# Optimization experiments

Hardware: AMD Instinct MI355X
Metric: run time of the kernel (lower is better)

## Reference

```python
import jax, jax.numpy as jnp
import numpy as np

N_USER = 100000
N_ITEM = 150000
N = N_USER + N_ITEM
D = 64            # latdim
NNZ = 1250000     # sparse adjacency nnz
BATCH = 16384     # node_ids batch
NUM_GNN_LAYERS = 2
GD = 16           # gate_dim (mamba d_model)
DSTATE = 8
DCONV = 4
EXPAND = 2
DINNER = GD * EXPAND  # 32
DTRANK = 1            # ceil(GD/16)
TEMP = 0.8            # gate_temp


def setup_inputs() -> dict:
    key = jax.random.key(0)
    ks = jax.random.split(key, 20)
    f32 = jnp.float32
    inp = {}
    inp["user_embedding"] = jax.random.normal(ks[0], (N_USER, D), f32) * 0.02
    inp["item_embedding"] = jax.random.normal(ks[1], (N_ITEM, D), f32) * 0.02
    inp["edge_row"] = jax.random.randint(ks[2], (NNZ,), 0, N, dtype=jnp.int32)
    inp["edge_col"] = jax.random.randint(ks[3], (NNZ,), 0, N, dtype=jnp.int32)
    inp["edge_val"] = jax.random.uniform(ks[4], (NNZ,), f32) * 0.1
    inp["node_ids"] = jax.random.randint(ks[5], (BATCH,), 0, N, dtype=jnp.int32)
    # gate params (torch Linear weight layout: [out, in])
    inp["down_w"] = jax.random.normal(ks[6], (GD, D), f32) * 0.02
    inp["in_proj_w"] = jax.random.normal(ks[7], (2 * DINNER, GD), f32) * 0.05
    inp["conv_w"] = jax.random.normal(ks[8], (DINNER, DCONV), f32) * 0.1
    inp["conv_b"] = jnp.zeros((DINNER,), f32)
    inp["x_proj_w"] = jax.random.normal(ks[9], (DTRANK + 2 * DSTATE, DINNER), f32) * 0.05
    inp["dt_proj_w"] = jax.random.normal(ks[10], (DINNER, DTRANK), f32) * 0.1
    inp["dt_proj_b"] = jax.random.normal(ks[11], (DINNER,), f32) * 0.1
    inp["A_log"] = jnp.log(jnp.broadcast_to(jnp.arange(1, DSTATE + 1, dtype=f32), (DINNER, DSTATE)))
    inp["D_param"] = jnp.ones((DINNER,), f32)
    inp["out_proj_w"] = jax.random.normal(ks[12], (GD, DINNER), f32) * 0.05
    inp["ln_g"] = jnp.ones((GD,), f32)
    inp["ln_b"] = jnp.zeros((GD,), f32)
    inp["to_logit_w"] = jax.random.normal(ks[13], (1, GD), f32) * 0.02
    inp["to_logit_b"] = jnp.zeros((1,), f32)
    return inp


def _mamba(g, in_proj_w, conv_w, conv_b, x_proj_w, dt_proj_w, dt_proj_b, A_log, D_param, out_proj_w):
    # g: [B, L, GD] -- standard Mamba block (selective scan)
    Bsz, L, _ = g.shape
    xz = g @ in_proj_w.T                     # [B,L,2*DINNER]
    x, z = jnp.split(xz, 2, axis=-1)         # each [B,L,DINNER]
    # causal depthwise conv1d along L (padding = DCONV-1, truncated to L)
    xp = jnp.pad(x, ((0, 0), (DCONV - 1, 0), (0, 0)))
    xconv = sum(xp[:, k:k + L, :] * conv_w[:, k] for k in range(DCONV)) + conv_b
    x = jax.nn.silu(xconv)
    dbc = x @ x_proj_w.T                     # [B,L,DTRANK+2*DSTATE]
    dt = dbc[..., :DTRANK]
    Bm = dbc[..., DTRANK:DTRANK + DSTATE]
    Cm = dbc[..., DTRANK + DSTATE:]
    dt = jax.nn.softplus(dt @ dt_proj_w.T + dt_proj_b)   # [B,L,DINNER]
    A = -jnp.exp(A_log)                                   # [DINNER,DSTATE]
    dA = jnp.exp(dt[..., None] * A)                       # [B,L,DINNER,DSTATE]
    dBx = dt[..., None] * Bm[:, :, None, :] * x[..., None]

    def step(h, ins):
        dA_t, dBx_t = ins
        h = dA_t * h + dBx_t
        return h, h

    h0 = jnp.zeros((Bsz, DINNER, DSTATE), x.dtype)
    _, hs = jax.lax.scan(step, h0, (jnp.swapaxes(dA, 0, 1), jnp.swapaxes(dBx, 0, 1)))
    hs = jnp.swapaxes(hs, 0, 1)                           # [B,L,DINNER,DSTATE]
    y = jnp.einsum('blds,bls->bld', hs, Cm) + D_param * x
    y = y * jax.nn.silu(z)
    return y @ out_proj_w.T                               # [B,L,GD]


def reference(user_embedding, item_embedding, edge_val, down_w, in_proj_w, conv_w,
              conv_b, x_proj_w, dt_proj_w, dt_proj_b, A_log, D_param, out_proj_w,
              ln_g, ln_b, to_logit_w, to_logit_b, edge_row, edge_col, node_ids):
    embeds = jnp.concatenate([user_embedding, item_embedding], axis=0)   # [N,D]
    seqs = [embeds[node_ids]]
    for _ in range(NUM_GNN_LAYERS):
        # sparse adjacency aggregation: out[r] += val * embeds[c]
        msg = edge_val[:, None] * embeds[edge_col]                       # [NNZ,D]
        embeds = jax.ops.segment_sum(msg, edge_row, num_segments=N)      # [N,D]
        # F.normalize(p=2, dim=1)
        nrm = jnp.linalg.norm(embeds, axis=1, keepdims=True)
        embeds = embeds / jnp.maximum(nrm, 1e-12)
        seqs.append(embeds[node_ids])
    seq = jnp.stack(seqs, axis=1)                                        # [B,L,D]

    # MambaDepthGating._compute_logits (deg_cond disabled)
    g = seq @ down_w.T                                                   # [B,L,GD]
    y = _mamba(g, in_proj_w, conv_w, conv_b, x_proj_w, dt_proj_w, dt_proj_b,
               A_log, D_param, out_proj_w)
    y = y + g
    mu = y.mean(-1, keepdims=True)
    var = y.var(-1, keepdims=True)
    y = (y - mu) / jnp.sqrt(var + 1e-12) * ln_g + ln_b                   # LN eps=1e-12
    logits = (y @ to_logit_w.T + to_logit_b)[..., 0]                     # [B,L]

    # fuse_from_logits, L=3 > 2 -> softmax path, perturbed=False
    w = jax.nn.softmax(logits / max(TEMP, 1e-6), axis=1)                 # [B,L]
    fused = jnp.sum(seq * w[..., None], axis=1)                          # [B,D]
    return fused
```

## Files before the change

### kernel.cpp

```cpp
#include <hip/hip_runtime.h>
#include <math.h>

#define N_USER 100000
#define N_ITEM 150000
#define NTOT   250000
#define D64    64
#define NNZ    1250000
#define BATCH  16384
#define GD     16
#define DSTATE 8
#define DCONV  4
#define DINNER 32
#define LSEQ   3
#define NBLK1  ((NTOT + 1023) >> 10)

__global__ void mark_nids_kernel(const int* __restrict__ nids,
                                 unsigned char* __restrict__ nidf,
                                 unsigned char* __restrict__ needf) {
    int b = blockIdx.x * 256 + threadIdx.x;
    if (b < BATCH) { int r = nids[b]; nidf[r] = 1; needf[r] = 1; }
}

__global__ void mark_need_kernel(const int* __restrict__ erow,
                                 const int* __restrict__ ecol,
                                 const unsigned char* __restrict__ nidf,
                                 unsigned char* __restrict__ needf) {
    int e = (blockIdx.x * 256 + threadIdx.x) * 4;
    if (e + 4 <= NNZ) {
        int4 r = *(const int4*)(erow + e);
        int4 c = *(const int4*)(ecol + e);
        if (nidf[r.x]) needf[c.x] = 1;
        if (nidf[r.y]) needf[c.y] = 1;
        if (nidf[r.z]) needf[c.z] = 1;
        if (nidf[r.w]) needf[c.w] = 1;
    } else {
        for (; e < NNZ; ++e) if (nidf[erow[e]]) needf[ecol[e]] = 1;
    }
}

__global__ void hist_slot_kernel(const int* __restrict__ erow,
                                 const unsigned char* __restrict__ needf,
                                 int* __restrict__ cnt, int* __restrict__ slot) {
    int e = (blockIdx.x * 256 + threadIdx.x) * 4;
    if (e + 4 <= NNZ) {
        int4 r = *(const int4*)(erow + e);
        if (needf[r.x]) slot[e + 0] = atomicAdd(&cnt[r.x], 1);
        if (needf[r.y]) slot[e + 1] = atomicAdd(&cnt[r.y], 1);
        if (needf[r.z]) slot[e + 2] = atomicAdd(&cnt[r.z], 1);
        if (needf[r.w]) slot[e + 3] = atomicAdd(&cnt[r.w], 1);
    } else {
        for (; e < NNZ; ++e) {
            int r = erow[e];
            if (needf[r]) slot[e] = atomicAdd(&cnt[r], 1);
        }
    }
}

__global__ __launch_bounds__(256) void scan1_kernel(const int* __restrict__ cnt,
                                                    const unsigned char* __restrict__ flags,
                                                    int* __restrict__ offs,
                                                    int* __restrict__ fpos,
                                                    int* __restrict__ bsum,
                                                    int* __restrict__ fbsum) {
    __shared__ int lds[256];
    __shared__ int lfs[256];
    int t = threadIdx.x;
    int base = (blockIdx.x << 10) + (t << 2);
    int d0 = (base + 0 < NTOT) ? cnt[base + 0] : 0;
    int d1 = (base + 1 < NTOT) ? cnt[base + 1] : 0;
    int d2 = (base + 2 < NTOT) ? cnt[base + 2] : 0;
    int d3 = (base + 3 < NTOT) ? cnt[base + 3] : 0;
    int f0 = (base + 0 < NTOT) ? (int)flags[base + 0] : 0;
    int f1 = (base + 1 < NTOT) ? (int)flags[base + 1] : 0;
    int f2 = (base + 2 < NTOT) ? (int)flags[base + 2] : 0;
    int f3 = (base + 3 < NTOT) ? (int)flags[base + 3] : 0;
    int s  = d0 + d1 + d2 + d3;
    int fs = f0 + f1 + f2 + f3;
    lds[t] = s; lfs[t] = fs;
    __syncthreads();
    for (int off = 1; off < 256; off <<= 1) {
        int v  = (t >= off) ? lds[t - off] : 0;
        int fv = (t >= off) ? lfs[t - off] : 0;
        __syncthreads();
        lds[t] += v; lfs[t] += fv;
        __syncthreads();
    }
    int excl  = lds[t] - s;
    int fexcl = lfs[t] - fs;
    if (base + 0 < NTOT) { offs[base + 0] = excl;                fpos[base + 0] = fexcl; }
    if (base + 1 < NTOT) { offs[base + 1] = excl + d0;           fpos[base + 1] = fexcl + f0; }
    if (base + 2 < NTOT) { offs[base + 2] = excl + d0 + d1;      fpos[base + 2] = fexcl + f0 + f1; }
    if (base + 3 < NTOT) { offs[base + 3] = excl + d0 + d1 + d2; fpos[base + 3] = fexcl + f0 + f1 + f2; }
    if (t == 255) { bsum[blockIdx.x] = lds[255]; fbsum[blockIdx.x] = lfs[255]; }
}

__global__ __launch_bounds__(256) void scan2_kernel(int* __restrict__ bsum,
                                                    int* __restrict__ fbsum) {
    __shared__ int lds[256];
    __shared__ int lfs[256];
    int t = threadIdx.x;
    int v0 = (t < NBLK1) ? bsum[t] : 0;
    int f0 = (t < NBLK1) ? fbsum[t] : 0;
    lds[t] = v0; lfs[t] = f0;
    __syncthreads();
    for (int off = 1; off < 256; off <<= 1) {
        int v  = (t >= off) ? lds[t - off] : 0;
        int fv = (t >= off) ? lfs[t - off] : 0;
        __syncthreads();
        lds[t] += v; lfs[t] += fv;
        __syncthreads();
    }
    if (t < NBLK1) { bsum[t] = lds[t] - v0; fbsum[t] = lfs[t] - f0; }
}

__global__ void scan3_kernel(int* __restrict__ offs, const int* __restrict__ bsum,
                             const int* __restrict__ cnt,
                             const int* __restrict__ fpos, const int* __restrict__ fbsum,
                             const unsigned char* __restrict__ flags,
                             int* __restrict__ row_list, int* __restrict__ nrows) {
    int i = blockIdx.x * 256 + threadIdx.x;
    if (i >= NTOT) return;
    int v = offs[i] + bsum[i >> 10];
    offs[i] = v;
    int fp = fpos[i] + fbsum[i >> 10];
    int fl = flags[i];
    if (fl) row_list[fp] = i;
    if (i == NTOT - 1) {
        offs[NTOT] = v + cnt[i];
        nrows[0] = fp + fl;
    }
}

__global__ void fill_kernel(const int* __restrict__ erow, const int* __restrict__ ecol,
                            const float* __restrict__ eval_, const int* __restrict__ offs,
                            const int* __restrict__ slot,
                            const unsigned char* __restrict__ needf,
                            int2* __restrict__ colval) {
    int e = (blockIdx.x * 256 + threadIdx.x) * 4;
    if (e + 4 <= NNZ) {
        int4   r = *(const int4*)(erow + e);
        int4   c = *(const int4*)(ecol + e);
        float4 v = *(const float4*)(eval_ + e);
        int4   s = *(const int4*)(slot + e);
        if (needf[r.x]) colval[offs[r.x] + s.x] = make_int2(c.x, __float_as_int(v.x));
        if (needf[r.y]) colval[offs[r.y] + s.y] = make_int2(c.y, __float_as_int(v.y));
        if (needf[r.z]) colval[offs[r.z] + s.z] = make_int2(c.z, __float_as_int(v.z));
        if (needf[r.w]) colval[offs[r.w] + s.w] = make_int2(c.w, __float_as_int(v.w));
    } else {
        for (; e < NNZ; ++e) {
            int r = erow[e];
            if (needf[r]) colval[offs[r] + slot[e]] = make_int2(ecol[e], __float_as_int(eval_[e]));
        }
    }
}

__global__ __launch_bounds__(256) void layer1_kernel(const float* __restrict__ user,
                                                     const float* __restrict__ item,
                                                     const int*  __restrict__ nrows,
                                                     const int*  __restrict__ row_list,
                                                     const int*  __restrict__ offs,
                                                     const int2* __restrict__ colval,
                                                     float* __restrict__ dst) {
    const float4* user4 = (const float4*)user;
    const float4* item4 = (const float4*)item;

    int gid    = (blockIdx.x << 4) + (threadIdx.x >> 4);
    int lane16 = threadIdx.x & 15;
    if (gid >= nrows[0]) return;
    int row = row_list[gid];
    int o0 = offs[row], o1 = offs[row + 1];

    float4 acc = make_float4(0.f, 0.f, 0.f, 0.f);
    int i = o0;
    for (; i + 4 <= o1; i += 4) {
        int2 cv0 = colval[i], cv1 = colval[i + 1], cv2 = colval[i + 2], cv3 = colval[i + 3];
        const float4* s0 = (cv0.x < N_USER) ? user4 + (size_t)cv0.x * 16
                                            : item4 + (size_t)(cv0.x - N_USER) * 16;
        const float4* s1 = (cv1.x < N_USER) ? user4 + (size_t)cv1.x * 16
                                            : item4 + (size_t)(cv1.x - N_USER) * 16;
        const float4* s2 = (cv2.x < N_USER) ? user4 + (size_t)cv2.x * 16
                                            : item4 + (size_t)(cv2.x - N_USER) * 16;
        const float4* s3 = (cv3.x < N_USER) ? user4 + (size_t)cv3.x * 16
                                            : item4 + (size_t)(cv3.x - N_USER) * 16;
        float4 v0 = s0[lane16], v1 = s1[lane16], v2 = s2[lane16], v3 = s3[lane16];
        float w0 = __int_as_float(cv0.y), w1 = __int_as_float(cv1.y);
        float w2 = __int_as_float(cv2.y), w3 = __int_as_float(cv3.y);
        acc.x = fmaf(w3, v3.x, fmaf(w2, v2.x, fmaf(w1, v1.x, fmaf(w0, v0.x, acc.x))));
        acc.y = fmaf(w3, v3.y, fmaf(w2, v2.y, fmaf(w1, v1.y, fmaf(w0, v0.y, acc.y))));
        acc.z = fmaf(w3, v3.z, fmaf(w2, v2.z, fmaf(w1, v1.z, fmaf(w0, v0.z, acc.z))));
        acc.w = fmaf(w3, v3.w, fmaf(w2, v2.w, fmaf(w1, v1.w, fmaf(w0, v0.w, acc.w))));
    }
    for (; i < o1; ++i) {
        int2 cv = colval[i];
        const float4* s0 = (cv.x < N_USER) ? user4 + (size_t)cv.x * 16
                                           : item4 + (size_t)(cv.x - N_USER) * 16;
        float4 v = s0[lane16];
        float w = __int_as_float(cv.y);
        acc.x = fmaf(w, v.x, acc.x);
        acc.y = fmaf(w, v.y, acc.y);
        acc.z = fmaf(w, v.z, acc.z);
        acc.w = fmaf(w, v.w, acc.w);
    }

    float s = fmaf(acc.x, acc.x, fmaf(acc.y, acc.y, fmaf(acc.z, acc.z, acc.w * acc.w)));
    #pragma unroll
    for (int m = 8; m >= 1; m >>= 1) s += __shfl_xor(s, m, 64);
    float scale = 1.f / fmaxf(sqrtf(s), 1e-12f);
    float4 r;
    r.x = acc.x * scale; r.y = acc.y * scale; r.z = acc.z * scale; r.w = acc.w * scale;
    ((float4*)dst)[(size_t)row * 16 + lane16] = r;
}

__global__ __launch_bounds__(256) void layer2_kernel(const float* __restrict__ embA,
                                                     const int*  __restrict__ nids,
                                                     const int*  __restrict__ offs,
                                                     const int2* __restrict__ colval,
                                                     float* __restrict__ embBc) {
    const float4* src4 = (const float4*)embA;
    int idx    = (blockIdx.x << 4) + (threadIdx.x >> 4);
    int lane16 = threadIdx.x & 15;
    if (idx >= BATCH) return;
    int row = nids[idx];
    int o0 = offs[row], o1 = offs[row + 1];

    float4 acc = make_float4(0.f, 0.f, 0.f, 0.f);
    int i = o0;
    for (; i + 4 <= o1; i += 4) {
        int2 cv0 = colval[i], cv1 = colval[i + 1], cv2 = colval[i + 2], cv3 = colval[i + 3];
        float4 v0 = src4[(size_t)cv0.x * 16 + lane16];
        float4 v1 = src4[(size_t)cv1.x * 16 + lane16];
        float4 v2 = src4[(size_t)cv2.x * 16 + lane16];
        float4 v3 = src4[(size_t)cv3.x * 16 + lane16];
        float w0 = __int_as_float(cv0.y), w1 = __int_as_float(cv1.y);
        float w2 = __int_as_float(cv2.y), w3 = __int_as_float(cv3.y);
        acc.x = fmaf(w3, v3.x, fmaf(w2, v2.x, fmaf(w1, v1.x, fmaf(w0, v0.x, acc.x))));
        acc.y = fmaf(w3, v3.y, fmaf(w2, v2.y, fmaf(w1, v1.y, fmaf(w0, v0.y, acc.y))));
        acc.z = fmaf(w3, v3.z, fmaf(w2, v2.z, fmaf(w1, v1.z, fmaf(w0, v0.z, acc.z))));
        acc.w = fmaf(w3, v3.w, fmaf(w2, v2.w, fmaf(w1, v1.w, fmaf(w0, v0.w, acc.w))));
    }
    for (; i < o1; ++i) {
        int2 cv = colval[i];
        float4 v = src4[(size_t)cv.x * 16 + lane16];
        float w = __int_as_float(cv.y);
        acc.x = fmaf(w, v.x, acc.x);
        acc.y = fmaf(w, v.y, acc.y);
        acc.z = fmaf(w, v.z, acc.z);
        acc.w = fmaf(w, v.w, acc.w);
    }

    float s = fmaf(acc.x, acc.x, fmaf(acc.y, acc.y, fmaf(acc.z, acc.z, acc.w * acc.w)));
    #pragma unroll
    for (int m = 8; m >= 1; m >>= 1) s += __shfl_xor(s, m, 64);
    float scale = 1.f / fmaxf(sqrtf(s), 1e-12f);
    float4 r;
    r.x = acc.x * scale; r.y = acc.y * scale; r.z = acc.z * scale; r.w = acc.w * scale;
    ((float4*)embBc)[(size_t)idx * 16 + lane16] = r;
}

__global__ __launch_bounds__(256) void final_kernel(
    const int*   __restrict__ nids,
    const float* __restrict__ user,      const float* __restrict__ item,
    const float* __restrict__ embA,      const float* __restrict__ embBc,
    const float* __restrict__ down_w,    const float* __restrict__ in_proj_w,
    const float* __restrict__ conv_w,    const float* __restrict__ conv_b,
    const float* __restrict__ x_proj_w,  const float* __restrict__ dt_proj_w,
    const float* __restrict__ dt_proj_b, const float* __restrict__ A_log,
    const float* __restrict__ D_param,   const float* __restrict__ out_proj_w,
    const float* __restrict__ ln_g,      const float* __restrict__ ln_b,
    const float* __restrict__ to_logit_w,const float* __restrict__ to_logit_b,
    float* __restrict__ out) {

    __shared__ float4 s_rows4[16 * 49];
    __shared__ float  s_downT[D64 * GD];
    __shared__ float  s_ipxT[GD * DINNER];
    __shared__ float  s_ipzT[GD * DINNER];
    __shared__ float  s_xpT[DINNER * 17];
    __shared__ float  s_opT[DINNER * GD];
    __shared__ float  s_AT[DSTATE * DINNER];
    __shared__ float4 s_cw4[DINNER];
    __shared__ float  s_cb[DINNER], s_dtw[DINNER], s_dtb[DINNER], s_Dp[DINNER];
    __shared__ float  s_lng[GD], s_lnb[GD], s_lw[GD];
    __shared__ float  s_lb;
    __shared__ float  s_g[16 * 49];
    __shared__ float  s_xs[16 * 98];
    __shared__ float  s_dbc[16 * 49];

    int t = threadIdx.x;

    for (int i = t; i < D64 * GD; i += 256) {
        int j = i & 15, d = i >> 4;
        s_downT[i] = down_w[j * D64 + d];
    }
    for (int i = t; i < GD * DINNER; i += 256) {
        int d = i & 31, j = i >> 5;
        s_ipxT[i] = in_proj_w[d * GD + j];
        s_ipzT[i] = in_proj_w[(d + DINNER) * GD + j];
    }
    for (int i = t; i < DINNER * 17; i += 256) {
        int d = i / 17, r = i % 17;
        s_xpT[i] = x_proj_w[r * DINNER + d];
    }
    for (int i = t; i < DINNER * GD; i += 256) {
        int j = i & 15, d = i >> 4;
        s_opT[i] = out_proj_w[j * DINNER + d];
    }
    for (int i = t; i < DSTATE * DINNER; i += 256) {
        int d = i & 31, s = i >> 5;
        s_AT[i] = -expf(A_log[d * DSTATE + s]);
    }
    if (t < DINNER) {
        s_cw4[t] = ((const float4*)conv_w)[t];
        s_cb[t] = conv_b[t]; s_dtw[t] = dt_proj_w[t];
        s_dtb[t] = dt_proj_b[t]; s_Dp[t] = D_param[t];
    }
    if (t < GD) { s_lng[t] = ln_g[t]; s_lnb[t] = ln_b[t]; s_lw[t] = to_logit_w[t]; }
    if (t == 0) s_lb = to_logit_b[0];

    int wave = t >> 6, lane = t & 63;
    int grp = lane >> 4, lane16 = lane & 15;
    int eb = wave * 4 + grp;
    int b  = blockIdx.x * 16 + eb;
    {
        int nid = nids[b];
        const float4* p0 = (const float4*)((nid < N_USER) ? user + (size_t)nid * D64
                                                          : item + (size_t)(nid - N_USER) * D64);
        const float4* p1 = (const float4*)(embA + (size_t)nid * D64);
        const float4* p2 = (const float4*)(embBc + (size_t)b * D64);
        s_rows4[eb * 49 + 0 * 16 + lane16] = p0[lane16];
        s_rows4[eb * 49 + 1 * 16 + lane16] = p1[lane16];
        s_rows4[eb * 49 + 2 * 16 + lane16] = p2[lane16];
    }
    __syncthreads();

    const float* rows = (const float*)s_rows4 + eb * 196;

    {
        float a0 = 0.f, a1 = 0.f, a2 = 0.f;
        #pragma unroll
        for (int d = 0; d < D64; ++d) {
            float w = s_downT[d * GD + lane16];
            a0 = fmaf(rows[d], w, a0);
            a1 = fmaf(rows[64 + d], w, a1);
            a2 = fmaf(rows[128 + d], w, a2);
        }
        s_g[eb * 49 + 0 * GD + lane16] = a0;
        s_g[eb * 49 + 1 * GD + lane16] = a1;
        s_g[eb * 49 + 2 * GD + lane16] = a2;
    }
    __syncthreads();

    const float* ge = s_g + eb * 49;

    float xsr[2][LSEQ];
    #pragma unroll
    for (int c = 0; c < 2; ++c) {
        int d = lane16 + 16 * c;
        float xl0 = 0.f, xl1 = 0.f, xl2 = 0.f;
        #pragma unroll
        for (int j = 0; j < GD; ++j) {
            float w = s_ipxT[j * DINNER + d];
            xl0 = fmaf(ge[j], w, xl0);
            xl1 = fmaf(ge[GD + j], w, xl1);
            xl2 = fmaf(ge[2 * GD + j], w, xl2);
        }
        float4 cw = s_cw4[d]; float cb = s_cb[d];
        float a0 = fmaf(xl0, cw.w, cb);
        float a1 = fmaf(xl1, cw.w, fmaf(xl0, cw.z, cb));
        float a2 = fmaf(xl2, cw.w, fmaf(xl1, cw.z, fmaf(xl0, cw.y, cb)));
        xsr[c][0] = a0 / (1.f + __expf(-a0));
        xsr[c][1] = a1 / (1.f + __expf(-a1));
        xsr[c][2] = a2 / (1.f + __expf(-a2));
        #pragma unroll
        for (int l = 0; l < LSEQ; ++l) s_xs[eb * 98 + l * DINNER + d] = xsr[c][l];
    }
    __syncthreads();

    {
        const float* xse = s_xs + eb * 98;
        int nr = (lane16 == 0) ? 2 : 1;
        for (int it = 0; it < nr; ++it) {
            int r = (it == 0) ? lane16 : 16;
            float a0 = 0.f, a1 = 0.f, a2 = 0.f;
            #pragma unroll
            for (int d = 0; d < DINNER; ++d) {
                float w = s_xpT[d * 17 + r];
                a0 = fmaf(xse[d], w, a0);
                a1 = fmaf(xse[DINNER + d], w, a1);
                a2 = fmaf(xse[2 * DINNER + d], w, a2);
            }
            s_dbc[eb * 49 + 0 * 17 + r] = a0;
            s_dbc[eb * 49 + 1 * 17 + r] = a1;
            s_dbc[eb * 49 + 2 * 17 + r] = a2;
        }
    }
    __syncthreads();

    {
        const float* dbce = s_dbc + eb * 49;
        float h[2][DSTATE];
        #pragma unroll
        for (int c = 0; c < 2; ++c)
            #pragma unroll
            for (int s = 0; s < DSTATE; ++s) h[c][s] = 0.f;
        #pragma unroll
        for (int l = 0; l < LSEQ; ++l) {
            float dtr = dbce[l * 17];
            float Bm[DSTATE], Cm[DSTATE];
            #pragma unroll
            for (int s = 0; s < DSTATE; ++s) {
                Bm[s] = dbce[l * 17 + 1 + s];
                Cm[s] = dbce[l * 17 + 9 + s];
            }
            #pragma unroll
            for (int c = 0; c < 2; ++c) {
                int d = lane16 + 16 * c;
                float pre = fmaf(dtr, s_dtw[d], s_dtb[d]);
                float dt  = (pre > 20.f) ? pre : __logf(1.f + __expf(pre));
                float xv  = xsr[c][l];
                float dtx = dt * xv;
                float acc = 0.f;
                #pragma unroll
                for (int s = 0; s < DSTATE; ++s) {
                    float dA = __expf(dt * s_AT[s * DINNER + d]);
                    h[c][s] = fmaf(dA, h[c][s], dtx * Bm[s]);
                    acc = fmaf(h[c][s], Cm[s], acc);
                }
                float y = fmaf(s_Dp[d], xv, acc);
                float zv = 0.f;
                #pragma unroll
                for (int j = 0; j < GD; ++j)
                    zv = fmaf(ge[l * GD + j], s_ipzT[j * DINNER + d], zv);
                float ys = y * (zv / (1.f + __expf(-zv)));
                s_xs[eb * 98 + l * DINNER + d] = ys;
            }
        }
    }
    __syncthreads();

    float lg[LSEQ];
    {
        const float* yse = s_xs + eb * 98;
        #pragma unroll
        for (int l = 0; l < LSEQ; ++l) {
            float a = 0.f;
            #pragma unroll
            for (int d = 0; d < DINNER; ++d)
                a = fmaf(yse[l * DINNER + d], s_opT[d * GD + lane16], a);
            float v = a + ge[l * GD + lane16];
            float sm = v, sq = v * v;
            #pragma unroll
            for (int m = 1; m <= 8; m <<= 1) {
                sm += __shfl_xor(sm, m, 64);
                sq += __shfl_xor(sq, m, 64);
            }
            float mu  = sm * (1.f / GD);
            float var = fmaxf(sq * (1.f / GD) - mu * mu, 0.f);
            float inv = rsqrtf(var + 1e-12f);
            float lo = fmaf(fmaf((v - mu) * inv, s_lng[lane16], s_lnb[lane16]),
                            s_lw[lane16], 0.f);
            #pragma unroll
            for (int m = 1; m <= 8; m <<= 1) lo += __shfl_xor(lo, m, 64);
            lg[l] = (lo + s_lb) * 1.25f;
        }
    }

    {
        float mx = fmaxf(lg[0], fmaxf(lg[1], lg[2]));
        float e0 = __expf(lg[0] - mx), e1 = __expf(lg[1] - mx), e2 = __expf(lg[2] - mx);
        float inv = 1.f / (e0 + e1 + e2);
        float w0 = e0 * inv, w1 = e1 * inv, w2 = e2 * inv;
        float4 r0 = s_rows4[eb * 49 + 0 * 16 + lane16];
        float4 r1 = s_rows4[eb * 49 + 1 * 16 + lane16];
        float4 r2 = s_rows4[eb * 49 + 2 * 16 + lane16];
        float4 r;
        r.x = w0 * r0.x + w1 * r1.x + w2 * r2.x;
        r.y = w0 * r0.y + w1 * r1.y + w2 * r2.y;
        r.z = w0 * r0.z + w1 * r1.z + w2 * r2.z;
        r.w = w0 * r0.w + w1 * r1.w + w2 * r2.w;
        ((float4*)out)[(size_t)b * 16 + lane16] = r;
    }
}

extern "C" void kernel_launch(void* const* d_in, const int* in_sizes, int n_in,
                              void* d_out, int out_size, void* d_ws, size_t ws_size,
                              hipStream_t stream) {
    const float* user      = (const float*)d_in[0];
    const float* item      = (const float*)d_in[1];
    const int*   erow      = (const int*)  d_in[2];
    const int*   ecol      = (const int*)  d_in[3];
    const float* eval_     = (const float*)d_in[4];
    const int*   nids      = (const int*)  d_in[5];
    const float* down_w    = (const float*)d_in[6];
    const float* in_proj_w = (const float*)d_in[7];
    const float* conv_w    = (const float*)d_in[8];
    const float* conv_b    = (const float*)d_in[9];
    const float* x_proj_w  = (const float*)d_in[10];
    const float* dt_proj_w = (const float*)d_in[11];
    const float* dt_proj_b = (const float*)d_in[12];
    const float* A_log     = (const float*)d_in[13];
    const float* D_param   = (const float*)d_in[14];
    const float* out_projw = (const float*)d_in[15];
    const float* ln_g      = (const float*)d_in[16];
    const float* ln_b      = (const float*)d_in[17];
    const float* to_lw     = (const float*)d_in[18];
    const float* to_lb     = (const float*)d_in[19];
    float* out = (float*)d_out;

    char* base = (char*)d_ws;
    float* embA  = (float*)base;
    float* embBc = (float*)(base + 64000000);
    char* c = base + 64000000 + 4194304;
    int* cnt   = (int*)c;
    unsigned char* nidf  = (unsigned char*)(c + 1000000);
    unsigned char* needf = (unsigned char*)(c + 1250000);
    size_t zbytes = 1500000;
    c += 1500032;
    int* nrows    = (int*)c;  c += 64;
    int* row_list = (int*)c;  c += (size_t)NTOT * 4;
    int* fpos     = (int*)c;  c += (size_t)NTOT * 4;
    int* offs     = (int*)c;  c += (size_t)(NTOT + 1) * 4 + 60;
    int* bsum     = (int*)c;  c += 1024;
    int* fbsum    = (int*)c;  c += 1024;
    int* slot     = (int*)c;  c += (size_t)NNZ * 4;
    int2* colval  = (int2*)c;

    hipMemsetAsync((void*)cnt, 0, zbytes, stream);

    mark_nids_kernel<<<(BATCH + 255) / 256, 256, 0, stream>>>(nids, nidf, needf);
    mark_need_kernel<<<(NNZ / 4 + 255) / 256, 256, 0, stream>>>(erow, ecol, nidf, needf);

    hist_slot_kernel<<<(NNZ / 4 + 255) / 256, 256, 0, stream>>>(erow, needf, cnt, slot);
    scan1_kernel<<<NBLK1, 256, 0, stream>>>(cnt, needf, offs, fpos, bsum, fbsum);
    scan2_kernel<<<1, 256, 0, stream>>>(bsum, fbsum);
    scan3_kernel<<<(NTOT + 255) / 256, 256, 0, stream>>>(offs, bsum, cnt, fpos, fbsum,
                                                         needf, row_list, nrows);
    fill_kernel<<<(NNZ / 4 + 255) / 256, 256, 0, stream>>>(erow, ecol, eval_, offs, slot,
                                                           needf, colval);

    layer1_kernel<<<(NTOT + 15) / 16, 256, 0, stream>>>(user, item, nrows, row_list, offs, colval, embA);
    layer2_kernel<<<BATCH / 16, 256, 0, stream>>>(embA, nids, offs, colval, embBc);

    final_kernel<<<BATCH / 16, 256, 0, stream>>>(nids, user, item, embA, embBc,
                                                 down_w, in_proj_w, conv_w, conv_b,
                                                 x_proj_w, dt_proj_w, dt_proj_b, A_log,
                                                 D_param, out_projw, ln_g, ln_b, to_lw, to_lb, out);
}
```

Before: 247.2 us.

## Fuse layer-2 gather into final kernel and build CSR with cursor atomics

The layer-2 SpMM gather and normalize for batch nodes now happen inside the final gating kernel, writing straight to shared memory. This removes the embBc intermediate and one kernel launch. CSR construction also changes: the histogram no longer records per-edge slots, and the fill pass claims positions with atomics on a per-row cursor copied from the offsets in the scan. This drops the slot array's write and read but adds a second round of atomics in the fill, and edge order within a row becomes nondeterministic, which can change float summation order.

New measurement: 247.7 us. No clear change (+0.2%).

```diff
diff --git a/kernel.cpp b/kernel.cpp
--- a/kernel.cpp
+++ b/kernel.cpp
@@ -38,20 +38,20 @@
     }
 }
 
-__global__ void hist_slot_kernel(const int* __restrict__ erow,
-                                 const unsigned char* __restrict__ needf,
-                                 int* __restrict__ cnt, int* __restrict__ slot) {
+__global__ void hist_kernel(const int* __restrict__ erow,
+                            const unsigned char* __restrict__ needf,
+                            int* __restrict__ cnt) {
     int e = (blockIdx.x * 256 + threadIdx.x) * 4;
     if (e + 4 <= NNZ) {
         int4 r = *(const int4*)(erow + e);
-        if (needf[r.x]) slot[e + 0] = atomicAdd(&cnt[r.x], 1);
-        if (needf[r.y]) slot[e + 1] = atomicAdd(&cnt[r.y], 1);
-        if (needf[r.z]) slot[e + 2] = atomicAdd(&cnt[r.z], 1);
-        if (needf[r.w]) slot[e + 3] = atomicAdd(&cnt[r.w], 1);
+        if (needf[r.x]) atomicAdd(&cnt[r.x], 1);
+        if (needf[r.y]) atomicAdd(&cnt[r.y], 1);
+        if (needf[r.z]) atomicAdd(&cnt[r.z], 1);
+        if (needf[r.w]) atomicAdd(&cnt[r.w], 1);
     } else {
         for (; e < NNZ; ++e) {
             int r = erow[e];
-            if (needf[r]) slot[e] = atomicAdd(&cnt[r], 1);
+            if (needf[r]) atomicAdd(&cnt[r], 1);
         }
     }
 }
@@ -117,11 +117,13 @@
                              const int* __restrict__ cnt,
                              const int* __restrict__ fpos, const int* __restrict__ fbsum,
                              const unsigned char* __restrict__ flags,
+                             int* __restrict__ cursor,
                              int* __restrict__ row_list, int* __restrict__ nrows) {
     int i = blockIdx.x * 256 + threadIdx.x;
     if (i >= NTOT) return;
     int v = offs[i] + bsum[i >> 10];
     offs[i] = v;
+    cursor[i] = v;
     int fp = fpos[i] + fbsum[i >> 10];
     int fl = flags[i];
     if (fl) row_list[fp] = i;
@@ -132,8 +134,8 @@
 }
 
 __global__ void fill_kernel(const int* __restrict__ erow, const int* __restrict__ ecol,
-                            const float* __restrict__ eval_, const int* __restrict__ offs,
-                            const int* __restrict__ slot,
+                            const float* __restrict__ eval_,
+                            int* __restrict__ cursor,
                             const unsigned char* __restrict__ needf,
                             int2* __restrict__ colval) {
     int e = (blockIdx.x * 256 + threadIdx.x) * 4;
@@ -141,15 +143,14 @@
         int4   r = *(const int4*)(erow + e);
         int4   c = *(const int4*)(ecol + e);
         float4 v = *(const float4*)(eval_ + e);
-        int4   s = *(const int4*)(slot + e);
-        if (needf[r.x]) colval[offs[r.x] + s.x] = make_int2(c.x, __float_as_int(v.x));
-        if (needf[r.y]) colval[offs[r.y] + s.y] = make_int2(c.y, __float_as_int(v.y));
-        if (needf[r.z]) colval[offs[r.z] + s.z] = make_int2(c.z, __float_as_int(v.z));
-        if (needf[r.w]) colval[offs[r.w] + s.w] = make_int2(c.w, __float_as_int(v.w));
+        if (needf[r.x]) colval[atomicAdd(&cursor[r.x], 1)] = make_int2(c.x, __float_as_int(v.x));
+        if (needf[r.y]) colval[atomicAdd(&cursor[r.y], 1)] = make_int2(c.y, __float_as_int(v.y));
+        if (needf[r.z]) colval[atomicAdd(&cursor[r.z], 1)] = make_int2(c.z, __float_as_int(v.z));
+        if (needf[r.w]) colval[atomicAdd(&cursor[r.w], 1)] = make_int2(c.w, __float_as_int(v.w));
     } else {
         for (; e < NNZ; ++e) {
             int r = erow[e];
-            if (needf[r]) colval[offs[r] + slot[e]] = make_int2(ecol[e], __float_as_int(eval_[e]));
+            if (needf[r]) colval[atomicAdd(&cursor[r], 1)] = make_int2(ecol[e], __float_as_int(eval_[e]));
         }
     }
 }
@@ -211,56 +212,11 @@
     ((float4*)dst)[(size_t)row * 16 + lane16] = r;
 }
 
-__global__ __launch_bounds__(256) void layer2_kernel(const float* __restrict__ embA,
-                                                     const int*  __restrict__ nids,
-                                                     const int*  __restrict__ offs,
-                                                     const int2* __restrict__ colval,
-                                                     float* __restrict__ embBc) {
-    const float4* src4 = (const float4*)embA;
-    int idx    = (blockIdx.x << 4) + (threadIdx.x >> 4);
-    int lane16 = threadIdx.x & 15;
-    if (idx >= BATCH) return;
-    int row = nids[idx];
-    int o0 = offs[row], o1 = offs[row + 1];
-
-    float4 acc = make_float4(0.f, 0.f, 0.f, 0.f);
-    int i = o0;
-    for (; i + 4 <= o1; i += 4) {
-        int2 cv0 = colval[i], cv1 = colval[i + 1], cv2 = colval[i + 2], cv3 = colval[i + 3];
-        float4 v0 = src4[(size_t)cv0.x * 16 + lane16];
-        float4 v1 = src4[(size_t)cv1.x * 16 + lane16];
-        float4 v2 = src4[(size_t)cv2.x * 16 + lane16];
-        float4 v3 = src4[(size_t)cv3.x * 16 + lane16];
-        float w0 = __int_as_float(cv0.y), w1 = __int_as_float(cv1.y);
-        float w2 = __int_as_float(cv2.y), w3 = __int_as_float(cv3.y);
-        acc.x = fmaf(w3, v3.x, fmaf(w2, v2.x, fmaf(w1, v1.x, fmaf(w0, v0.x, acc.x))));
-        acc.y = fmaf(w3, v3.y, fmaf(w2, v2.y, fmaf(w1, v1.y, fmaf(w0, v0.y, acc.y))));
-        acc.z = fmaf(w3, v3.z, fmaf(w2, v2.z, fmaf(w1, v1.z, fmaf(w0, v0.z, acc.z))));
-        acc.w = fmaf(w3, v3.w, fmaf(w2, v2.w, fmaf(w1, v1.w, fmaf(w0, v0.w, acc.w))));
-    }
-    for (; i < o1; ++i) {
-        int2 cv = colval[i];
-        float4 v = src4[(size_t)cv.x * 16 + lane16];
-        float w = __int_as_float(cv.y);
-        acc.x = fmaf(w, v.x, acc.x);
-        acc.y = fmaf(w, v.y, acc.y);
-        acc.z = fmaf(w, v.z, acc.z);
-        acc.w = fmaf(w, v.w, acc.w);
-    }
-
-    float s = fmaf(acc.x, acc.x, fmaf(acc.y, acc.y, fmaf(acc.z, acc.z, acc.w * acc.w)));
-    #pragma unroll
-    for (int m = 8; m >= 1; m >>= 1) s += __shfl_xor(s, m, 64);
-    float scale = 1.f / fmaxf(sqrtf(s), 1e-12f);
-    float4 r;
-    r.x = acc.x * scale; r.y = acc.y * scale; r.z = acc.z * scale; r.w = acc.w * scale;
-    ((float4*)embBc)[(size_t)idx * 16 + lane16] = r;
-}
-
 __global__ __launch_bounds__(256) void final_kernel(
     const int*   __restrict__ nids,
     const float* __restrict__ user,      const float* __restrict__ item,
-    const float* __restrict__ embA,      const float* __restrict__ embBc,
+    const float* __restrict__ embA,
+    const int*   __restrict__ offs,      const int2* __restrict__ colval,
     const float* __restrict__ down_w,    const float* __restrict__ in_proj_w,
     const float* __restrict__ conv_w,    const float* __restrict__ conv_b,
     const float* __restrict__ x_proj_w,  const float* __restrict__ dt_proj_w,
@@ -286,6 +242,53 @@
     __shared__ float  s_dbc[16 * 49];
 
     int t = threadIdx.x;
+    int wave = t >> 6, lane = t & 63;
+    int grp = lane >> 4, lane16 = lane & 15;
+    int eb = wave * 4 + grp;
+    int b  = blockIdx.x * 16 + eb;
+    int nid = nids[b];
+
+    {
+        const float4* p0 = (const float4*)((nid < N_USER) ? user + (size_t)nid * D64
+                                                          : item + (size_t)(nid - N_USER) * D64);
+        const float4* p1 = (const float4*)(embA + (size_t)nid * D64);
+        s_rows4[eb * 49 + 0 * 16 + lane16] = p0[lane16];
+        s_rows4[eb * 49 + 1 * 16 + lane16] = p1[lane16];
+
+        const float4* src4 = (const float4*)embA;
+        int o0 = offs[nid], o1 = offs[nid + 1];
+        float4 acc = make_float4(0.f, 0.f, 0.f, 0.f);
+        int i = o0;
+        for (; i + 4 <= o1; i += 4) {
+            int2 cv0 = colval[i], cv1 = colval[i + 1], cv2 = colval[i + 2], cv3 = colval[i + 3];
+            float4 v0 = src4[(size_t)cv0.x * 16 + lane16];
+            float4 v1 = src4[(size_t)cv1.x * 16 + lane16];
+            float4 v2 = src4[(size_t)cv2.x * 16 + lane16];
+            float4 v3 = src4[(size_t)cv3.x * 16 + lane16];
+            float w0 = __int_as_float(cv0.y), w1 = __int_as_float(cv1.y);
+            float w2 = __int_as_float(cv2.y), w3 = __int_as_float(cv3.y);
+            acc.x = fmaf(w3, v3.x, fmaf(w2, v2.x, fmaf(w1, v1.x, fmaf(w0, v0.x, acc.x))));
+            acc.y = fmaf(w3, v3.y, fmaf(w2, v2.y, fmaf(w1, v1.y, fmaf(w0, v0.y, acc.y))));
+            acc.z = fmaf(w3, v3.z, fmaf(w2, v2.z, fmaf(w1, v1.z, fmaf(w0, v0.z, acc.z))));
+            acc.w = fmaf(w3, v3.w, fmaf(w2, v2.w, fmaf(w1, v1.w, fmaf(w0, v0.w, acc.w))));
+        }
+        for (; i < o1; ++i) {
+            int2 cv = colval[i];
+            float4 v = src4[(size_t)cv.x * 16 + lane16];
+            float w = __int_as_float(cv.y);
+            acc.x = fmaf(w, v.x, acc.x);
+            acc.y = fmaf(w, v.y, acc.y);
+            acc.z = fmaf(w, v.z, acc.z);
+            acc.w = fmaf(w, v.w, acc.w);
+        }
+        float s = fmaf(acc.x, acc.x, fmaf(acc.y, acc.y, fmaf(acc.z, acc.z, acc.w * acc.w)));
+        #pragma unroll
+        for (int m = 8; m >= 1; m >>= 1) s += __shfl_xor(s, m, 64);
+        float scale = 1.f / fmaxf(sqrtf(s), 1e-12f);
+        float4 r;
+        r.x = acc.x * scale; r.y = acc.y * scale; r.z = acc.z * scale; r.w = acc.w * scale;
+        s_rows4[eb * 49 + 2 * 16 + lane16] = r;
+    }
 
     for (int i = t; i < D64 * GD; i += 256) {
         int j = i & 15, d = i >> 4;
@@ -315,21 +318,6 @@
     }
     if (t < GD) { s_lng[t] = ln_g[t]; s_lnb[t] = ln_b[t]; s_lw[t] = to_logit_w[t]; }
     if (t == 0) s_lb = to_logit_b[0];
-
-    int wave = t >> 6, lane = t & 63;
-    int grp = lane >> 4, lane16 = lane & 15;
-    int eb = wave * 4 + grp;
-    int b  = blockIdx.x * 16 + eb;
-    {
-        int nid = nids[b];
-        const float4* p0 = (const float4*)((nid < N_USER) ? user + (size_t)nid * D64
-                                                          : item + (size_t)(nid - N_USER) * D64);
-        const float4* p1 = (const float4*)(embA + (size_t)nid * D64);
-        const float4* p2 = (const float4*)(embBc + (size_t)b * D64);
-        s_rows4[eb * 49 + 0 * 16 + lane16] = p0[lane16];
-        s_rows4[eb * 49 + 1 * 16 + lane16] = p1[lane16];
-        s_rows4[eb * 49 + 2 * 16 + lane16] = p2[lane16];
-    }
     __syncthreads();
 
     const float* rows = (const float*)s_rows4 + eb * 196;
@@ -507,9 +495,8 @@
     float* out = (float*)d_out;
 
     char* base = (char*)d_ws;
-    float* embA  = (float*)base;
-    float* embBc = (float*)(base + 64000000);
-    char* c = base + 64000000 + 4194304;
+    float* embA = (float*)base;
+    char* c = base + 64000000;
     int* cnt   = (int*)c;
     unsigned char* nidf  = (unsigned char*)(c + 1000000);
     unsigned char* needf = (unsigned char*)(c + 1250000);
@@ -518,10 +505,10 @@
     int* nrows    = (int*)c;  c += 64;
     int* row_list = (int*)c;  c += (size_t)NTOT * 4;
     int* fpos     = (int*)c;  c += (size_t)NTOT * 4;
+    int* cursor   = (int*)c;  c += (size_t)NTOT * 4;
     int* offs     = (int*)c;  c += (size_t)(NTOT + 1) * 4 + 60;
     int* bsum     = (int*)c;  c += 1024;
     int* fbsum    = (int*)c;  c += 1024;
-    int* slot     = (int*)c;  c += (size_t)NNZ * 4;
     int2* colval  = (int2*)c;
 
     hipMemsetAsync((void*)cnt, 0, zbytes, stream);
@@ -529,18 +516,17 @@
     mark_nids_kernel<<<(BATCH + 255) / 256, 256, 0, stream>>>(nids, nidf, needf);
     mark_need_kernel<<<(NNZ / 4 + 255) / 256, 256, 0, stream>>>(erow, ecol, nidf, needf);
 
-    hist_slot_kernel<<<(NNZ / 4 + 255) / 256, 256, 0, stream>>>(erow, needf, cnt, slot);
+    hist_kernel<<<(NNZ / 4 + 255) / 256, 256, 0, stream>>>(erow, needf, cnt);
     scan1_kernel<<<NBLK1, 256, 0, stream>>>(cnt, needf, offs, fpos, bsum, fbsum);
     scan2_kernel<<<1, 256, 0, stream>>>(bsum, fbsum);
     scan3_kernel<<<(NTOT + 255) / 256, 256, 0, stream>>>(offs, bsum, cnt, fpos, fbsum,
-                                                         needf, row_list, nrows);
-    fill_kernel<<<(NNZ / 4 + 255) / 256, 256, 0, stream>>>(erow, ecol, eval_, offs, slot,
+                                                         needf, cursor, row_list, nrows);
+    fill_kernel<<<(NNZ / 4 + 255) / 256, 256, 0, stream>>>(erow, ecol, eval_, cursor,
                                                            needf, colval);
 
     layer1_kernel<<<(NTOT + 15) / 16, 256, 0, stream>>>(user, item, nrows, row_list, offs, colval, embA);
-    layer2_kernel<<<BATCH / 16, 256, 0, stream>>>(embA, nids, offs, colval, embBc);
-
-    final_kernel<<<BATCH / 16, 256, 0, stream>>>(nids, user, item, embA, embBc,
+
+    final_kernel<<<BATCH / 16, 256, 0, stream>>>(nids, user, item, embA, offs, colval,
                                                  down_w, in_proj_w, conv_w, conv_b,
                                                  x_proj_w, dt_proj_w, dt_proj_b, A_log,
                                                  D_param, out_projw, ln_g, ln_b, to_lw, to_lb, out);
```
